# Optimization experiments

Hardware: AMD Instinct MI355X
Metric: run time of the kernel (lower is better)

## Reference

```python
import jax, jax.numpy as jnp
import numpy as np


def setup_inputs() -> dict:
    key = jax.random.key(0)
    k1, k2, k3 = jax.random.split(key, 3)
    B, T, D, P = 4, 4096, 512, 4096
    inputs = jax.random.normal(k1, (B, T, D), dtype=jnp.float32)
    # xavier_uniform-like scale for param tokens
    bound = float(np.sqrt(6.0 / (P + D)))
    key_tokens = jax.random.uniform(k2, (P, D), dtype=jnp.float32, minval=-bound, maxval=bound)
    value_tokens = jax.random.uniform(k3, (P, D), dtype=jnp.float32, minval=-bound, maxval=bound)
    return {"inputs": inputs, "key_tokens": key_tokens, "value_tokens": value_tokens}


def reference(inputs, key_tokens, value_tokens):
    # attn_weight: [B, T, P]
    attn = jnp.einsum('btd,pd->btp', inputs, key_tokens)
    # gelu_l2_norm activation: exact GELU, then row-wise L2 norm over param-token dim, scaled by sqrt(P)
    a = jax.nn.gelu(attn, approximate=False)
    scale = jnp.sqrt(jnp.asarray(a.shape[-1], dtype=a.dtype))
    a = a / jnp.linalg.norm(a, axis=-1, keepdims=True) * scale
    # dropout_p = 0.0 -> identity
    return jnp.einsum('btp,pv->btv', a, value_tokens)
```

## Files before the change

### kernel.cpp

```cpp
#include <hip/hip_runtime.h>
#include <hip/hip_bf16.h>


typedef __attribute__((ext_vector_type(8))) short bf16x8;
typedef __attribute__((ext_vector_type(4))) float f32x4;

static constexpr int M_TOTAL = 16384;
static constexpr int DDIM    = 512;
static constexpr int PDIM    = 4096;
static constexpr int BM      = 64;
static constexpr int BP      = 64;
static constexpr int GPAD    = 72;

#define AS1C(p) ((const __attribute__((address_space(1))) void*)(p))
#define AS3(p)  ((__attribute__((address_space(3))) void*)(p))

__device__ __forceinline__ unsigned short f2bf(float f) {
    union { float f; unsigned u; } v; v.f = f;
    unsigned r = v.u + 0x7FFFu + ((v.u >> 16) & 1u);
    return (unsigned short)(r >> 16);
}

__device__ __forceinline__ float gelu_f(float x) {
    float t2 = 2.0f * x * (0.7978845608028654f + 0.035677408136300125f * x * x);
    return x / (1.0f + __expf(-t2));
}

__global__ void conv_k(const float* __restrict__ kin, unsigned short* __restrict__ kbf) {
    int i = (blockIdx.x * 256 + threadIdx.x) * 4;
    float4 v = *reinterpret_cast<const float4*>(kin + i);
    ushort4 o;
    o.x = f2bf(v.x); o.y = f2bf(v.y); o.z = f2bf(v.z); o.w = f2bf(v.w);
    *reinterpret_cast<ushort4*>(kbf + i) = o;
}

__global__ void conv_vt2(const float* __restrict__ vin, unsigned short* __restrict__ vt2) {
    int tid  = blockIdx.x * 256 + threadIdx.x;
    int lane = tid & 63;
    int blk  = tid >> 6;
    int nb = blk & 31;
    int pb = blk >> 5;
    int p0 = pb * 32 + ((lane >> 4) << 3);
    int n  = nb * 16 + (lane & 15);
    ushort4 a, b;
    a.x = f2bf(vin[(p0 + 0) * DDIM + n]);
    a.y = f2bf(vin[(p0 + 1) * DDIM + n]);
    a.z = f2bf(vin[(p0 + 2) * DDIM + n]);
    a.w = f2bf(vin[(p0 + 3) * DDIM + n]);
    b.x = f2bf(vin[(p0 + 4) * DDIM + n]);
    b.y = f2bf(vin[(p0 + 5) * DDIM + n]);
    b.z = f2bf(vin[(p0 + 6) * DDIM + n]);
    b.w = f2bf(vin[(p0 + 7) * DDIM + n]);
    *reinterpret_cast<ushort4*>(vt2 + tid * 8 + 0) = a;
    *reinterpret_cast<ushort4*>(vt2 + tid * 8 + 4) = b;
}

__global__ __launch_bounds__(512, 1) void fused_pattn(
    const float* __restrict__ x,
    const unsigned short* __restrict__ kbf,
    const unsigned short* __restrict__ vt2,
    float* __restrict__ out)
{
    __shared__ unsigned short k_lds[2][BM * DDIM];
    __shared__ unsigned short g_lds[2][BM * GPAD];
    __shared__ float ss_lds[BM];

    const int tid  = threadIdx.x;
    const int lane = tid & 63;
    const int w    = tid >> 6;
    const int l15  = lane & 15;
    const int l4   = lane >> 4;
    const int m_base = blockIdx.x * BM;

    if (tid < BM) ss_lds[tid] = 0.0f;

    if (w < 4) {
        const int mg = w >> 1;
        const int pg = w & 1;

        #pragma unroll
        for (int i = 0; i < 16; ++i) {
            int r = w * 16 + i;
            const unsigned short* src = kbf + (size_t)r * DDIM + ((lane ^ (i & 7)) << 3);
            __builtin_amdgcn_global_load_lds(AS1C(src), AS3(&k_lds[0][r * DDIM]), 16, 0, 0);
        }

        bf16x8 xf0[16], xf1[16];
        #pragma unroll
        for (int mb = 0; mb < 2; ++mb) {
            const float* xrow = x + (size_t)(m_base + mg * 32 + mb * 16 + l15) * DDIM + l4 * 8;
            #pragma unroll
            for (int db = 0; db < 16; ++db) {
                float4 a = *reinterpret_cast<const float4*>(xrow + db * 32);
                float4 bq = *reinterpret_cast<const float4*>(xrow + db * 32 + 4);
                bf16x8 f;
                f[0] = (short)f2bf(a.x);  f[1] = (short)f2bf(a.y);
                f[2] = (short)f2bf(a.z);  f[3] = (short)f2bf(a.w);
                f[4] = (short)f2bf(bq.x); f[5] = (short)f2bf(bq.y);
                f[6] = (short)f2bf(bq.z); f[7] = (short)f2bf(bq.w);
                if (mb == 0) xf0[db] = f; else xf1[db] = f;
            }
        }
        asm volatile("s_waitcnt vmcnt(0)" ::: "memory");
        __builtin_amdgcn_s_barrier();

        f32x4 zero4 = {0.0f, 0.0f, 0.0f, 0.0f};
        float ss[2] = {0.0f, 0.0f};
        const int swz = (l15 & 7) << 3;

        #pragma unroll 1
        for (int t = 0; t < PDIM / BP; ++t) {
            {
                const int P0n = ((t + 1) & 63) * BP;
                #pragma unroll
                for (int i = 0; i < 16; ++i) {
                    int r = w * 16 + i;
                    const unsigned short* src =
                        kbf + (size_t)(P0n + r) * DDIM + ((lane ^ (i & 7)) << 3);
                    __builtin_amdgcn_global_load_lds(
                        AS1C(src), AS3(&k_lds[(t + 1) & 1][r * DDIM]), 16, 0, 0);
                }
            }

            f32x4 sacc00 = zero4, sacc01 = zero4, sacc10 = zero4, sacc11 = zero4;
            const unsigned short* kb = &k_lds[t & 1][0];
            __builtin_amdgcn_s_setprio(1);
            #pragma unroll
            for (int db = 0; db < 16; ++db) {
                int cole = ((db << 5) | (l4 << 3)) ^ swz;
                bf16x8 kv0 = *reinterpret_cast<const bf16x8*>(
                    kb + (pg * 32 + l15) * DDIM + cole);
                bf16x8 kv1 = *reinterpret_cast<const bf16x8*>(
                    kb + (pg * 32 + 16 + l15) * DDIM + cole);
                sacc00 = __builtin_amdgcn_mfma_f32_16x16x32_bf16(kv0, xf0[db], sacc00, 0, 0, 0);
                sacc01 = __builtin_amdgcn_mfma_f32_16x16x32_bf16(kv0, xf1[db], sacc01, 0, 0, 0);
                sacc10 = __builtin_amdgcn_mfma_f32_16x16x32_bf16(kv1, xf0[db], sacc10, 0, 0, 0);
                sacc11 = __builtin_amdgcn_mfma_f32_16x16x32_bf16(kv1, xf1[db], sacc11, 0, 0, 0);
            }
            __builtin_amdgcn_s_setprio(0);

            unsigned short* gb = &g_lds[t & 1][0];
            #pragma unroll
            for (int pf = 0; pf < 2; ++pf) {
                #pragma unroll
                for (int mb = 0; mb < 2; ++mb) {
                    f32x4 sv = (pf == 0) ? (mb == 0 ? sacc00 : sacc01)
                                         : (mb == 0 ? sacc10 : sacc11);
                    float g0 = gelu_f(sv[0]);
                    float g1 = gelu_f(sv[1]);
                    float g2 = gelu_f(sv[2]);
                    float g3 = gelu_f(sv[3]);
                    ss[mb] += g0 * g0 + g1 * g1 + g2 * g2 + g3 * g3;
                    unsigned d0 = (unsigned)f2bf(g0) | ((unsigned)f2bf(g1) << 16);
                    unsigned d1 = (unsigned)f2bf(g2) | ((unsigned)f2bf(g3) << 16);
                    int m_l = mg * 32 + mb * 16 + l15;
                    int p_l = pg * 32 + pf * 16 + l4 * 4;
                    *reinterpret_cast<uint2*>(&gb[m_l * GPAD + p_l]) = make_uint2(d0, d1);
                }
            }
            asm volatile("s_waitcnt lgkmcnt(0)" ::: "memory");
            asm volatile("s_waitcnt vmcnt(0)" ::: "memory");
            __builtin_amdgcn_s_barrier();
        }

        #pragma unroll
        for (int mb = 0; mb < 2; ++mb) {
            float v = ss[mb];
            v += __shfl_xor(v, 16, 64);
            v += __shfl_xor(v, 32, 64);
            if (l4 == 0) atomicAdd(&ss_lds[mg * 32 + mb * 16 + l15], v);
        }
        asm volatile("s_waitcnt lgkmcnt(0)" ::: "memory");
        __builtin_amdgcn_s_barrier();
    } else {
        const int bw = w - 4;

        bf16x8 bg[16];
        #pragma unroll
        for (int ks = 0; ks < 2; ++ks)
            #pragma unroll
            for (int nf = 0; nf < 8; ++nf)
                bg[ks * 8 + nf] = *reinterpret_cast<const bf16x8*>(
                    vt2 + ((size_t)(ks * 32 + bw * 8 + nf) * 64 + lane) * 8);

        f32x4 zero4 = {0.0f, 0.0f, 0.0f, 0.0f};
        f32x4 oacc[4][8];
        #pragma unroll
        for (int i = 0; i < 4; ++i)
            #pragma unroll
            for (int j = 0; j < 8; ++j) oacc[i][j] = zero4;

        __builtin_amdgcn_s_barrier();

        #pragma unroll 1
        for (int t = 0; t < PDIM / BP; ++t) {
            __builtin_amdgcn_s_barrier();

            const unsigned short* gb = &g_lds[t & 1][0];
            __builtin_amdgcn_s_setprio(1);
            #pragma unroll
            for (int ks = 0; ks < 2; ++ks) {
                bf16x8 ag[4];
                #pragma unroll
                for (int mf = 0; mf < 4; ++mf)
                    ag[mf] = *reinterpret_cast<const bf16x8*>(
                        &gb[(mf * 16 + l15) * GPAD + ks * 32 + l4 * 8]);
                #pragma unroll
                for (int mf = 0; mf < 4; ++mf)
                    #pragma unroll
                    for (int nf = 0; nf < 8; ++nf)
                        oacc[mf][nf] = __builtin_amdgcn_mfma_f32_16x16x32_bf16(
                            ag[mf], bg[ks * 8 + nf], oacc[mf][nf], 0, 0, 0);
            }
            __builtin_amdgcn_s_setprio(0);

            {
                const int pb0 = ((t + 1) & 63) * 2;
                #pragma unroll
                for (int ks = 0; ks < 2; ++ks)
                    #pragma unroll
                    for (int nf = 0; nf < 8; ++nf)
                        bg[ks * 8 + nf] = *reinterpret_cast<const bf16x8*>(
                            vt2 + ((size_t)((pb0 + ks) * 32 + bw * 8 + nf) * 64 + lane) * 8);
            }
        }

        __builtin_amdgcn_s_barrier();

        #pragma unroll
        for (int mf = 0; mf < 4; ++mf) {
            #pragma unroll
            for (int r = 0; r < 4; ++r) {
                int m_l = mf * 16 + l4 * 4 + r;
                float scale = 64.0f * rsqrtf(ss_lds[m_l]);
                float* orow = out + (size_t)(m_base + m_l) * DDIM + bw * 128 + l15;
                #pragma unroll
                for (int nf = 0; nf < 8; ++nf)
                    orow[nf * 16] = oacc[mf][nf][r] * scale;
            }
        }
    }
}

extern "C" void kernel_launch(void* const* d_in, const int* in_sizes, int n_in,
                              void* d_out, int out_size, void* d_ws, size_t ws_size,
                              hipStream_t stream) {
    const float* x = (const float*)d_in[0];
    const float* k = (const float*)d_in[1];
    const float* v = (const float*)d_in[2];
    float* out = (float*)d_out;

    unsigned short* kbf = (unsigned short*)d_ws;
    unsigned short* vt2 = kbf + (size_t)PDIM * DDIM;

    conv_k  <<<dim3(2048), dim3(256), 0, stream>>>(k, kbf);
    conv_vt2<<<dim3(1024), dim3(256), 0, stream>>>(v, vt2);
    fused_pattn<<<dim3(M_TOTAL / BM), dim3(512), 0, stream>>>(x, kbf, vt2, out);
}
```

Before: 190.7 us.

## Shrink producer to two waves with x fragments in AGPRs

The producer side of the warp-specialized kernel drops from four waves to two. Each producer wave now computes a 32x64 score tile with eight MFMAs per d-step instead of four. The x operand is held in AGPRs through inline asm MFMA to relieve VGPR pressure, and the LDS atomicAdd for row sums becomes a plain store since each row now has a single owner. The block shrinks to 384 threads, which frees resources, but it doubles per-wave producer work and the GELU cost, so the producer may become the bottleneck for the four consumer waves.

```diff
diff --git a/kernel.cpp b/kernel.cpp
--- a/kernel.cpp
+++ b/kernel.cpp
@@ -3,6 +3,7 @@
 
 
 typedef __attribute__((ext_vector_type(8))) short bf16x8;
+typedef __attribute__((ext_vector_type(4))) int   i32x4;
 typedef __attribute__((ext_vector_type(4))) float f32x4;
 
 static constexpr int M_TOTAL = 16384;
@@ -10,27 +11,34 @@
 static constexpr int PDIM    = 4096;
 static constexpr int BM      = 64;
 static constexpr int BP      = 64;
+static constexpr int NSLOT   = PDIM / BP;
 static constexpr int GPAD    = 72;
 
 #define AS1C(p) ((const __attribute__((address_space(1))) void*)(p))
 #define AS3(p)  ((__attribute__((address_space(3))) void*)(p))
 
-__device__ __forceinline__ unsigned short f2bf(float f) {
+__device__ __forceinline__ unsigned f2bf(float f) {
     union { float f; unsigned u; } v; v.f = f;
     unsigned r = v.u + 0x7FFFu + ((v.u >> 16) & 1u);
-    return (unsigned short)(r >> 16);
+    return (r >> 16);
 }
 
 __device__ __forceinline__ float gelu_f(float x) {
     float t2 = 2.0f * x * (0.7978845608028654f + 0.035677408136300125f * x * x);
     return x / (1.0f + __expf(-t2));
+}
+
+__device__ __forceinline__ void mfma_av(f32x4& d, const i32x4& kv, const i32x4& xf) {
+    asm("v_mfma_f32_16x16x32_bf16 %0, %1, %2, %0"
+        : "+v"(d) : "v"(kv), "a"(xf));
 }
 
 __global__ void conv_k(const float* __restrict__ kin, unsigned short* __restrict__ kbf) {
     int i = (blockIdx.x * 256 + threadIdx.x) * 4;
     float4 v = *reinterpret_cast<const float4*>(kin + i);
     ushort4 o;
-    o.x = f2bf(v.x); o.y = f2bf(v.y); o.z = f2bf(v.z); o.w = f2bf(v.w);
+    o.x = (unsigned short)f2bf(v.x); o.y = (unsigned short)f2bf(v.y);
+    o.z = (unsigned short)f2bf(v.z); o.w = (unsigned short)f2bf(v.w);
     *reinterpret_cast<ushort4*>(kbf + i) = o;
 }
 
@@ -43,25 +51,25 @@
     int p0 = pb * 32 + ((lane >> 4) << 3);
     int n  = nb * 16 + (lane & 15);
     ushort4 a, b;
-    a.x = f2bf(vin[(p0 + 0) * DDIM + n]);
-    a.y = f2bf(vin[(p0 + 1) * DDIM + n]);
-    a.z = f2bf(vin[(p0 + 2) * DDIM + n]);
-    a.w = f2bf(vin[(p0 + 3) * DDIM + n]);
-    b.x = f2bf(vin[(p0 + 4) * DDIM + n]);
-    b.y = f2bf(vin[(p0 + 5) * DDIM + n]);
-    b.z = f2bf(vin[(p0 + 6) * DDIM + n]);
-    b.w = f2bf(vin[(p0 + 7) * DDIM + n]);
+    a.x = (unsigned short)f2bf(vin[(p0 + 0) * DDIM + n]);
+    a.y = (unsigned short)f2bf(vin[(p0 + 1) * DDIM + n]);
+    a.z = (unsigned short)f2bf(vin[(p0 + 2) * DDIM + n]);
+    a.w = (unsigned short)f2bf(vin[(p0 + 3) * DDIM + n]);
+    b.x = (unsigned short)f2bf(vin[(p0 + 4) * DDIM + n]);
+    b.y = (unsigned short)f2bf(vin[(p0 + 5) * DDIM + n]);
+    b.z = (unsigned short)f2bf(vin[(p0 + 6) * DDIM + n]);
+    b.w = (unsigned short)f2bf(vin[(p0 + 7) * DDIM + n]);
     *reinterpret_cast<ushort4*>(vt2 + tid * 8 + 0) = a;
     *reinterpret_cast<ushort4*>(vt2 + tid * 8 + 4) = b;
 }
 
-__global__ __launch_bounds__(512, 1) void fused_pattn(
+__global__ __launch_bounds__(384, 1) void fused_pattn(
     const float* __restrict__ x,
     const unsigned short* __restrict__ kbf,
     const unsigned short* __restrict__ vt2,
     float* __restrict__ out)
 {
-    __shared__ unsigned short k_lds[2][BM * DDIM];
+    __shared__ unsigned short k_lds[2][BP * DDIM];
     __shared__ unsigned short g_lds[2][BM * GPAD];
     __shared__ float ss_lds[BM];
 
@@ -72,33 +80,29 @@
     const int l4   = lane >> 4;
     const int m_base = blockIdx.x * BM;
 
-    if (tid < BM) ss_lds[tid] = 0.0f;
-
-    if (w < 4) {
-        const int mg = w >> 1;
-        const int pg = w & 1;
-
-        #pragma unroll
-        for (int i = 0; i < 16; ++i) {
-            int r = w * 16 + i;
+    if (w < 2) {
+
+        #pragma unroll
+        for (int i = 0; i < 32; ++i) {
+            int r = w * 32 + i;
             const unsigned short* src = kbf + (size_t)r * DDIM + ((lane ^ (i & 7)) << 3);
             __builtin_amdgcn_global_load_lds(AS1C(src), AS3(&k_lds[0][r * DDIM]), 16, 0, 0);
         }
 
-        bf16x8 xf0[16], xf1[16];
+        i32x4 xa0[16], xa1[16];
         #pragma unroll
         for (int mb = 0; mb < 2; ++mb) {
-            const float* xrow = x + (size_t)(m_base + mg * 32 + mb * 16 + l15) * DDIM + l4 * 8;
+            const float* xrow = x + (size_t)(m_base + w * 32 + mb * 16 + l15) * DDIM + l4 * 8;
             #pragma unroll
             for (int db = 0; db < 16; ++db) {
-                float4 a = *reinterpret_cast<const float4*>(xrow + db * 32);
+                float4 a  = *reinterpret_cast<const float4*>(xrow + db * 32);
                 float4 bq = *reinterpret_cast<const float4*>(xrow + db * 32 + 4);
-                bf16x8 f;
-                f[0] = (short)f2bf(a.x);  f[1] = (short)f2bf(a.y);
-                f[2] = (short)f2bf(a.z);  f[3] = (short)f2bf(a.w);
-                f[4] = (short)f2bf(bq.x); f[5] = (short)f2bf(bq.y);
-                f[6] = (short)f2bf(bq.z); f[7] = (short)f2bf(bq.w);
-                if (mb == 0) xf0[db] = f; else xf1[db] = f;
+                i32x4 f;
+                f[0] = (int)(f2bf(a.x)  | (f2bf(a.y)  << 16));
+                f[1] = (int)(f2bf(a.z)  | (f2bf(a.w)  << 16));
+                f[2] = (int)(f2bf(bq.x) | (f2bf(bq.y) << 16));
+                f[3] = (int)(f2bf(bq.z) | (f2bf(bq.w) << 16));
+                if (mb == 0) xa0[db] = f; else xa1[db] = f;
             }
         }
         asm volatile("s_waitcnt vmcnt(0)" ::: "memory");
@@ -109,12 +113,12 @@
         const int swz = (l15 & 7) << 3;
 
         #pragma unroll 1
-        for (int t = 0; t < PDIM / BP; ++t) {
+        for (int t = 0; t < NSLOT; ++t) {
             {
-                const int P0n = ((t + 1) & 63) * BP;
-                #pragma unroll
-                for (int i = 0; i < 16; ++i) {
-                    int r = w * 16 + i;
+                const int P0n = ((t + 1) & (NSLOT - 1)) * BP;
+                #pragma unroll
+                for (int i = 0; i < 32; ++i) {
+                    int r = w * 32 + i;
                     const unsigned short* src =
                         kbf + (size_t)(P0n + r) * DDIM + ((lane ^ (i & 7)) << 3);
                     __builtin_amdgcn_global_load_lds(
@@ -122,39 +126,41 @@
                 }
             }
 
-            f32x4 sacc00 = zero4, sacc01 = zero4, sacc10 = zero4, sacc11 = zero4;
+            f32x4 sacc[2][4];
+            #pragma unroll
+            for (int mb = 0; mb < 2; ++mb)
+                #pragma unroll
+                for (int pf = 0; pf < 4; ++pf) sacc[mb][pf] = zero4;
             const unsigned short* kb = &k_lds[t & 1][0];
             __builtin_amdgcn_s_setprio(1);
             #pragma unroll
             for (int db = 0; db < 16; ++db) {
                 int cole = ((db << 5) | (l4 << 3)) ^ swz;
-                bf16x8 kv0 = *reinterpret_cast<const bf16x8*>(
-                    kb + (pg * 32 + l15) * DDIM + cole);
-                bf16x8 kv1 = *reinterpret_cast<const bf16x8*>(
-                    kb + (pg * 32 + 16 + l15) * DDIM + cole);
-                sacc00 = __builtin_amdgcn_mfma_f32_16x16x32_bf16(kv0, xf0[db], sacc00, 0, 0, 0);
-                sacc01 = __builtin_amdgcn_mfma_f32_16x16x32_bf16(kv0, xf1[db], sacc01, 0, 0, 0);
-                sacc10 = __builtin_amdgcn_mfma_f32_16x16x32_bf16(kv1, xf0[db], sacc10, 0, 0, 0);
-                sacc11 = __builtin_amdgcn_mfma_f32_16x16x32_bf16(kv1, xf1[db], sacc11, 0, 0, 0);
+                i32x4 kv0 = *reinterpret_cast<const i32x4*>(kb + (l15)      * DDIM + cole);
+                i32x4 kv1 = *reinterpret_cast<const i32x4*>(kb + (16 + l15) * DDIM + cole);
+                i32x4 kv2 = *reinterpret_cast<const i32x4*>(kb + (32 + l15) * DDIM + cole);
+                i32x4 kv3 = *reinterpret_cast<const i32x4*>(kb + (48 + l15) * DDIM + cole);
+                mfma_av(sacc[0][0], kv0, xa0[db]);  mfma_av(sacc[1][0], kv0, xa1[db]);
+                mfma_av(sacc[0][1], kv1, xa0[db]);  mfma_av(sacc[1][1], kv1, xa1[db]);
+                mfma_av(sacc[0][2], kv2, xa0[db]);  mfma_av(sacc[1][2], kv2, xa1[db]);
+                mfma_av(sacc[0][3], kv3, xa0[db]);  mfma_av(sacc[1][3], kv3, xa1[db]);
             }
             __builtin_amdgcn_s_setprio(0);
 
             unsigned short* gb = &g_lds[t & 1][0];
             #pragma unroll
-            for (int pf = 0; pf < 2; ++pf) {
-                #pragma unroll
-                for (int mb = 0; mb < 2; ++mb) {
-                    f32x4 sv = (pf == 0) ? (mb == 0 ? sacc00 : sacc01)
-                                         : (mb == 0 ? sacc10 : sacc11);
-                    float g0 = gelu_f(sv[0]);
-                    float g1 = gelu_f(sv[1]);
-                    float g2 = gelu_f(sv[2]);
-                    float g3 = gelu_f(sv[3]);
+            for (int mb = 0; mb < 2; ++mb) {
+                const int m_l = w * 32 + mb * 16 + l15;
+                #pragma unroll
+                for (int pf = 0; pf < 4; ++pf) {
+                    float g0 = gelu_f(sacc[mb][pf][0]);
+                    float g1 = gelu_f(sacc[mb][pf][1]);
+                    float g2 = gelu_f(sacc[mb][pf][2]);
+                    float g3 = gelu_f(sacc[mb][pf][3]);
                     ss[mb] += g0 * g0 + g1 * g1 + g2 * g2 + g3 * g3;
-                    unsigned d0 = (unsigned)f2bf(g0) | ((unsigned)f2bf(g1) << 16);
-                    unsigned d1 = (unsigned)f2bf(g2) | ((unsigned)f2bf(g3) << 16);
-                    int m_l = mg * 32 + mb * 16 + l15;
-                    int p_l = pg * 32 + pf * 16 + l4 * 4;
+                    unsigned d0 = f2bf(g0) | (f2bf(g1) << 16);
+                    unsigned d1 = f2bf(g2) | (f2bf(g3) << 16);
+                    int p_l = pf * 16 + l4 * 4;
                     *reinterpret_cast<uint2*>(&gb[m_l * GPAD + p_l]) = make_uint2(d0, d1);
                 }
             }
@@ -168,12 +174,12 @@
             float v = ss[mb];
             v += __shfl_xor(v, 16, 64);
             v += __shfl_xor(v, 32, 64);
-            if (l4 == 0) atomicAdd(&ss_lds[mg * 32 + mb * 16 + l15], v);
+            if (l4 == 0) ss_lds[w * 32 + mb * 16 + l15] = v;
         }
         asm volatile("s_waitcnt lgkmcnt(0)" ::: "memory");
         __builtin_amdgcn_s_barrier();
     } else {
-        const int bw = w - 4;
+        const int bw = w - 2;
 
         bf16x8 bg[16];
         #pragma unroll
@@ -193,7 +199,7 @@
         __builtin_amdgcn_s_barrier();
 
         #pragma unroll 1
-        for (int t = 0; t < PDIM / BP; ++t) {
+        for (int t = 0; t < NSLOT; ++t) {
             __builtin_amdgcn_s_barrier();
 
             const unsigned short* gb = &g_lds[t & 1][0];
@@ -215,7 +221,7 @@
             __builtin_amdgcn_s_setprio(0);
 
             {
-                const int pb0 = ((t + 1) & 63) * 2;
+                const int pb0 = ((t + 1) & (NSLOT - 1)) * 2;
                 #pragma unroll
                 for (int ks = 0; ks < 2; ++ks)
                     #pragma unroll
@@ -255,5 +261,5 @@
 
     conv_k  <<<dim3(2048), dim3(256), 0, stream>>>(k, kbf);
     conv_vt2<<<dim3(1024), dim3(256), 0, stream>>>(v, vt2);
-    fused_pattn<<<dim3(M_TOTAL / BM), dim3(512), 0, stream>>>(x, kbf, vt2, out);
-}
+    fused_pattn<<<dim3(M_TOTAL / BM), dim3(384), 0, stream>>>(x, kbf, vt2, out);
+}
```

Result: slower. 290.0 us (+52.1%).
